# Performance work log

Hardware: AMD Instinct MI355X
Metric: run time of the kernel (lower is better)

Reference implementation:

```python
import jax, jax.numpy as jnp
import numpy as np

N = 20000
E = 320000
D_IN = 3
HID = 256
HEADS = 4
C = HID // HEADS  # per-head channels = 64
LAYERS = 3
NUM_GRAPHS = 64
LN_EPS = 1e-5
NEG_SLOPE = 0.2


def setup_inputs() -> dict:
    key = jax.random.key(0)
    ks = jax.random.split(key, 12)
    x = jax.random.normal(ks[0], (N, D_IN), dtype=jnp.float32)
    edge_index = jax.random.randint(ks[1], (2, E), 0, N, dtype=jnp.int64)
    batch = jnp.sort(jax.random.randint(ks[2], (N,), 0, NUM_GRAPHS, dtype=jnp.int64))
    s = 0.05
    W_emb = jax.random.normal(ks[3], (D_IN, HID), dtype=jnp.float32) * s
    b_emb = jnp.zeros((HID,), dtype=jnp.float32)
    W_gat = jax.random.normal(ks[4], (LAYERS, HID, HID), dtype=jnp.float32) * s
    att_src = jax.random.normal(ks[5], (LAYERS, HEADS, C), dtype=jnp.float32) * s
    att_dst = jax.random.normal(ks[6], (LAYERS, HEADS, C), dtype=jnp.float32) * s
    b_gat = jnp.zeros((LAYERS, HID), dtype=jnp.float32)
    ln_g = jnp.ones((LAYERS, HID), dtype=jnp.float32)
    ln_b = jnp.zeros((LAYERS, HID), dtype=jnp.float32)
    return {"x": x, "edge_index": edge_index, "batch": batch,
            "W_emb": W_emb, "b_emb": b_emb, "W_gat": W_gat,
            "att_src": att_src, "att_dst": att_dst, "b_gat": b_gat,
            "ln_g": ln_g, "ln_b": ln_b}


def _layer_norm(h, g, b):
    mu = jnp.mean(h, axis=-1, keepdims=True)
    var = jnp.var(h, axis=-1, keepdims=True)
    return (h - mu) * jax.lax.rsqrt(var + LN_EPS) * g + b


def _gat_layer(h, src, dst, loop_mask, Wl, a_s, a_d, bl):
    # h: [N, HID] -> per-head features [N, H, C]
    hp = (h @ Wl).reshape(N, HEADS, C)
    alpha_s = jnp.einsum('nhc,hc->nh', hp, a_s)   # [N, H]
    alpha_d = jnp.einsum('nhc,hc->nh', hp, a_d)   # [N, H]
    # edges + self-loops; pre-existing self-loops masked out (PyG removes then re-adds)
    e = jax.nn.leaky_relu(alpha_s[src] + alpha_d[dst], NEG_SLOPE)  # [E+N, H]
    e = jnp.where(loop_mask[:, None], -jnp.inf, e)
    # segment softmax over destination neighborhoods
    m = jax.ops.segment_max(e, dst, num_segments=N)
    ex = jnp.exp(e - m[dst])
    denom = jax.ops.segment_sum(ex, dst, num_segments=N)
    alpha = ex / jnp.maximum(denom[dst], 1e-16)    # [E+N, H]
    # weighted scatter-add of source features
    out = jax.ops.segment_sum(alpha[:, :, None] * hp[src], dst, num_segments=N)  # [N,H,C]
    return out.reshape(N, HID) + bl, alpha


def reference(x, edge_index, batch, W_emb, b_emb, W_gat, att_src, att_dst, b_gat, ln_g, ln_b):
    src0 = edge_index[0]
    dst0 = edge_index[1]
    loop_ids = jnp.arange(N, dtype=src0.dtype)
    src = jnp.concatenate([src0, loop_ids])
    dst = jnp.concatenate([dst0, loop_ids])
    loop_mask = jnp.concatenate([src0 == dst0, jnp.zeros((N,), dtype=bool)])

    h = x @ W_emb + b_emb  # node embedding
    attns = []
    for l in range(LAYERS):
        h, alpha = _gat_layer(h, src, dst, loop_mask, W_gat[l], att_src[l], att_dst[l], b_gat[l])
        h = _layer_norm(h, ln_g[l], ln_b[l])
        attns.append(alpha)
        # dropout is identity in eval mode
    # global mean pool over graphs
    sums = jax.ops.segment_sum(h, batch, num_segments=NUM_GRAPHS)
    cnts = jax.ops.segment_sum(jnp.ones((N,), dtype=h.dtype), batch, num_segments=NUM_GRAPHS)
    graph_repr = sums / jnp.maximum(cnts, 1.0)[:, None]
    return h, graph_repr, jnp.stack(attns)
```

## Files before the change

### kernel.cpp

```cpp
#include <hip/hip_runtime.h>
#include <hip/hip_bf16.h>

#define N_NODES 20000
#define E_EDGES 320000
#define HID 256
#define HEADS 4
#define CPH 64
#define LAYERS 3
#define NGRAPH 64
#define LN_EPS 1e-5f
#define NEG 0.2f
#define MAXD 256

__device__ __forceinline__ float lrelu_f(float v){ return v > 0.f ? v : NEG*v; }

__global__ __launch_bounds__(256) void k_cvt_f(const int* __restrict__ raw,
                                               int* __restrict__ src, int* __restrict__ dst){
  int e = blockIdx.x*256 + threadIdx.x;
  if (e >= E_EDGES) return;
  src[e] = raw[e];
  dst[e] = raw[E_EDGES + e];
}

__global__ __launch_bounds__(256) void k_embed_f(const float* __restrict__ x, const float* __restrict__ W,
                                                 const float* __restrict__ b, float* __restrict__ h){
  int n = blockIdx.x; int c = threadIdx.x;
  float x0 = x[n*3+0], x1 = x[n*3+1], x2 = x[n*3+2];
  h[(size_t)n*HID+c] = fmaf(x0, W[c], fmaf(x1, W[HID+c], fmaf(x2, W[2*HID+c], b[c])));
}

__global__ void k_hist_f(const int* __restrict__ dst, int* __restrict__ deg){
  int e = blockIdx.x*256 + threadIdx.x;
  if (e < E_EDGES) atomicAdd(&deg[dst[e]], 1);
}

__global__ __launch_bounds__(256) void k_scan_f(const int* __restrict__ deg, int* __restrict__ rp, int* __restrict__ cur){
  __shared__ int part[256];
  const int CH = (N_NODES + 255)/256;
  int t = threadIdx.x;
  int s = 0;
  for (int i=0;i<CH;i++){ int idx=t*CH+i; if (idx<N_NODES) s += deg[idx]; }
  part[t]=s; __syncthreads();
  for (int off=1; off<256; off<<=1){
    int v = (t>=off) ? part[t-off] : 0; __syncthreads();
    part[t]+=v; __syncthreads();
  }
  int run = (t==0) ? 0 : part[t-1];
  for (int i=0;i<CH;i++){ int idx=t*CH+i; if (idx<N_NODES){ rp[idx]=run; cur[idx]=run; run+=deg[idx]; } }
  if (t==255) rp[N_NODES]=run;
}

__global__ void k_scatter_f(const int* __restrict__ src, const int* __restrict__ dst, int* __restrict__ cur,
                            int* __restrict__ csrc, int* __restrict__ ceid){
  int e = blockIdx.x*256 + threadIdx.x;
  if (e < E_EDGES){
    int d = dst[e];
    int pos = atomicAdd(&cur[d],1);
    csrc[pos] = src[e];
    ceid[pos] = e;
  }
}

__global__ __launch_bounds__(256) void k_gemm_f(const float* __restrict__ A, const float* __restrict__ B,
                                                float* __restrict__ C, int M){
  __shared__ float sA[64][68];
  __shared__ float sB[64][68];
  int r0 = blockIdx.x*64, c0 = blockIdx.y*64;
  int tid = threadIdx.x, tx = tid&15, ty = tid>>4;
  float acc[4][4] = {};
  for (int k0=0; k0<HID; k0+=64){
    #pragma unroll
    for (int i=0;i<4;i++){
      int slot = tid + i*256;
      int rr = slot>>4, kk = (slot&15)<<2;
      int gr = r0+rr; if (gr >= M) gr = M-1;
      float4 va = *(const float4*)(A + (size_t)gr*HID + k0 + kk);
      sA[kk+0][rr]=va.x; sA[kk+1][rr]=va.y; sA[kk+2][rr]=va.z; sA[kk+3][rr]=va.w;
      float4 vb = *(const float4*)(B + (size_t)(k0+rr)*HID + c0 + kk);
      sB[rr][kk+0]=vb.x; sB[rr][kk+1]=vb.y; sB[rr][kk+2]=vb.z; sB[rr][kk+3]=vb.w;
    }
    __syncthreads();
    #pragma unroll 8
    for (int k=0;k<64;k++){
      float4 a4 = *(const float4*)&sA[k][ty*4];
      float4 b4 = *(const float4*)&sB[k][tx*4];
      float av[4]={a4.x,a4.y,a4.z,a4.w}, bv[4]={b4.x,b4.y,b4.z,b4.w};
      #pragma unroll
      for (int i=0;i<4;i++)
        #pragma unroll
        for (int j=0;j<4;j++) acc[i][j] = fmaf(av[i], bv[j], acc[i][j]);
    }
    __syncthreads();
  }
  #pragma unroll
  for (int i=0;i<4;i++){
    int r = r0 + ty*4 + i;
    if (r < M){
      float4 o = {acc[i][0],acc[i][1],acc[i][2],acc[i][3]};
      *(float4*)(C + (size_t)r*HID + c0 + tx*4) = o;
    }
  }
}

__global__ __launch_bounds__(64) void k_alpha_f(const float* __restrict__ hp, const float* __restrict__ as_w,
                                                const float* __restrict__ ad_w,
                                                float* __restrict__ asn, float* __restrict__ adn){
  int n = blockIdx.x, lane = threadIdx.x;
  #pragma unroll
  for (int h=0; h<HEADS; h++){
    float v = hp[(size_t)n*HID + h*CPH + lane];
    float ps = v * as_w[h*CPH + lane];
    float pd = v * ad_w[h*CPH + lane];
    #pragma unroll
    for (int off=32; off; off>>=1){ ps += __shfl_xor(ps, off, 64); pd += __shfl_xor(pd, off, 64); }
    if (lane == 0){ asn[n*HEADS+h] = ps; adn[n*HEADS+h] = pd; }
  }
}

__global__ __launch_bounds__(64) void k_aggr_f(const float* __restrict__ hp, const float* __restrict__ asn,
                                               const float* __restrict__ adn, const int* __restrict__ rp,
                                               const int* __restrict__ csrc, const int* __restrict__ ceid,
                                               const float* __restrict__ bl, const float* __restrict__ lg,
                                               const float* __restrict__ lb, float* __restrict__ hout,
                                               float* __restrict__ attn,
                                               float* __restrict__ hOut32){
  __shared__ float ps[MAXD][HEADS];
  int n = blockIdx.x, lane = threadIdx.x;
  int beg = rp[n];
  int cnt = rp[n+1] - beg;
  float ad[HEADS], es[HEADS];
  #pragma unroll
  for (int h=0;h<HEADS;h++){
    ad[h]=adn[n*HEADS+h];
    es[h]=lrelu_f(asn[n*HEADS+h]+ad[h]);
  }
  float dp[HEADS] = {0.f,0.f,0.f,0.f};
  for (int j=lane; j<cnt; j+=64){
    int s = csrc[beg+j];
    #pragma unroll
    for (int h=0;h<HEADS;h++){
      float p = 0.f;
      if (s != n) p = __expf(lrelu_f(asn[s*HEADS+h]+ad[h]));
      if (j < MAXD) ps[j][h] = p;
      dp[h] += p;
    }
  }
  #pragma unroll
  for (int h=0;h<HEADS;h++){
    #pragma unroll
    for (int off=32; off; off>>=1) dp[h] += __shfl_xor(dp[h], off, 64);
  }
  float slf[HEADS], inv[HEADS];
  #pragma unroll
  for (int h=0;h<HEADS;h++){
    slf[h] = __expf(es[h]);
    inv[h] = 1.f / fmaxf(dp[h] + slf[h], 1e-16f);
  }
  __syncthreads();
  for (int j=lane; j<cnt; j+=64){
    int s = csrc[beg+j];
    size_t eid = (size_t)ceid[beg+j];
    #pragma unroll
    for (int h=0;h<HEADS;h++){
      float p = (j < MAXD) ? ps[j][h]
              : ((s!=n) ? __expf(lrelu_f(asn[s*HEADS+h]+ad[h])) : 0.f);
      attn[eid*HEADS + h] = p * inv[h];
    }
  }
  if (lane==0){
    #pragma unroll
    for (int h=0;h<HEADS;h++)
      attn[(size_t)(E_EDGES+n)*HEADS + h] = slf[h]*inv[h];
  }
  float acc[HEADS];
  #pragma unroll
  for (int h=0;h<HEADS;h++) acc[h] = slf[h]*hp[(size_t)n*HID + h*CPH + lane];
  for (int j=0;j<cnt;j++){
    int s = csrc[beg+j];
    if (j < MAXD){
      #pragma unroll
      for (int h=0;h<HEADS;h++)
        acc[h] = fmaf(ps[j][h], hp[(size_t)s*HID + h*CPH + lane], acc[h]);
    } else if (s != n){
      #pragma unroll
      for (int h=0;h<HEADS;h++){
        float p = __expf(lrelu_f(asn[s*HEADS+h]+ad[h]));
        acc[h] = fmaf(p, hp[(size_t)s*HID + h*CPH + lane], acc[h]);
      }
    }
  }
  float o[HEADS], sum=0.f, sq=0.f;
  #pragma unroll
  for (int h=0;h<HEADS;h++){
    o[h] = fmaf(acc[h], inv[h], bl[h*CPH+lane]);
    sum += o[h]; sq = fmaf(o[h],o[h],sq);
  }
  #pragma unroll
  for (int off=32; off; off>>=1){ sum += __shfl_xor(sum,off,64); sq += __shfl_xor(sq,off,64); }
  float mu = sum * (1.f/HID);
  float var = sq*(1.f/HID) - mu*mu;
  float rs = rsqrtf(var + LN_EPS);
  #pragma unroll
  for (int h=0;h<HEADS;h++){
    int c = h*CPH+lane;
    float y = (o[h]-mu)*rs*lg[c] + lb[c];
    hout[(size_t)n*HID + c] = y;
    if (hOut32) hOut32[(size_t)n*HID + c] = y;
  }
}

__global__ __launch_bounds__(256) void k_pool1(const float* __restrict__ h, const int* __restrict__ batch,
                                               float* __restrict__ gracc){
  const int nb = 2048;
  const int chunk = (N_NODES + nb - 1)/nb;
  int n0 = blockIdx.x*chunk;
  int n1 = n0 + chunk; if (n1 > N_NODES) n1 = N_NODES;
  if (n0 >= n1) return;
  int c = threadIdx.x;
  float acc = 0.f; int curg = -1;
  for (int n=n0; n<n1; ++n){
    int g = batch[n];
    if (g != curg){
      if (curg >= 0) atomicAdd(&gracc[curg*HID+c], acc);
      curg = g; acc = 0.f;
    }
    acc += h[(size_t)n*HID + c];
  }
  if (curg >= 0) atomicAdd(&gracc[curg*HID+c], acc);
}

__global__ __launch_bounds__(256) void k_pool2(const float* __restrict__ gracc, const int* __restrict__ batch,
                                               float* __restrict__ out_gr){
  int g = blockIdx.x, c = threadIdx.x;
  int lo=0, hi=N_NODES;
  while (lo<hi){ int mid=(lo+hi)>>1; if (batch[mid] < g) lo=mid+1; else hi=mid; }
  int start = lo;
  lo=start; hi=N_NODES;
  while (lo<hi){ int mid=(lo+hi)>>1; if (batch[mid] < g+1) lo=mid+1; else hi=mid; }
  float cnt = (float)(lo - start);
  out_gr[g*HID + c] = gracc[g*HID + c] / fmaxf(cnt, 1.f);
}

extern "C" void kernel_launch(void* const* d_in, const int* in_sizes, int n_in,
                              void* d_out, int out_size, void* d_ws, size_t ws_size,
                              hipStream_t stream){
  const float* x     = (const float*)d_in[0];
  const int*   ei    = (const int*)d_in[1];
  const int*   batch = (const int*)d_in[2];
  const float* W_emb = (const float*)d_in[3];
  const float* b_emb = (const float*)d_in[4];
  const float* W_gat = (const float*)d_in[5];
  const float* att_s = (const float*)d_in[6];
  const float* att_d = (const float*)d_in[7];
  const float* b_gat = (const float*)d_in[8];
  const float* ln_g  = (const float*)d_in[9];
  const float* ln_b  = (const float*)d_in[10];

  float* out     = (float*)d_out;
  float* out_h   = out;
  float* out_gr  = out + (size_t)N_NODES*HID;
  float* out_att = out_gr + (size_t)NGRAPH*HID;

  char* ws = (char*)d_ws;
  size_t off = 0;
  auto alloc = [&](size_t bytes){ void* p = ws + off; off += (bytes + 255) & ~size_t(255); return p; };
  float* h_cur = (float*)alloc((size_t)N_NODES*HID*4);
  float* hp    = (float*)alloc((size_t)N_NODES*HID*4);
  float* asn   = (float*)alloc((size_t)N_NODES*HEADS*4);
  float* adn   = (float*)alloc((size_t)N_NODES*HEADS*4);
  int* deg     = (int*)alloc((size_t)N_NODES*4);
  int* rp      = (int*)alloc((size_t)(N_NODES+1)*4);
  int* cur     = (int*)alloc((size_t)N_NODES*4);
  int* csrc    = (int*)alloc((size_t)E_EDGES*4);
  int* ceid    = (int*)alloc((size_t)E_EDGES*4);
  int* srcA    = (int*)alloc((size_t)E_EDGES*4);
  int* dstA    = (int*)alloc((size_t)E_EDGES*4);
  float* gracc = (float*)alloc((size_t)NGRAPH*HID*4);

  hipMemsetAsync(deg, 0, (size_t)N_NODES*4, stream);
  hipMemsetAsync(gracc, 0, (size_t)NGRAPH*HID*4, stream);

  k_cvt_f    <<<(E_EDGES+255)/256, 256, 0, stream>>>(ei, srcA, dstA);
  k_hist_f   <<<(E_EDGES+255)/256, 256, 0, stream>>>(dstA, deg);
  k_scan_f   <<<1, 256, 0, stream>>>(deg, rp, cur);
  k_scatter_f<<<(E_EDGES+255)/256, 256, 0, stream>>>(srcA, dstA, cur, csrc, ceid);

  k_embed_f  <<<N_NODES, 256, 0, stream>>>(x, W_emb, b_emb, h_cur);

  dim3 ggrid((N_NODES+63)/64, HID/64);
  for (int l=0; l<LAYERS; ++l){
    k_gemm_f <<<ggrid, 256, 0, stream>>>(h_cur, W_gat + (size_t)l*HID*HID, hp, N_NODES);
    k_alpha_f<<<N_NODES, 64, 0, stream>>>(hp, att_s + l*HEADS*CPH, att_d + l*HEADS*CPH, asn, adn);
    k_aggr_f <<<N_NODES, 64, 0, stream>>>(hp, asn, adn, rp, csrc, ceid,
              b_gat + l*HID, ln_g + l*HID, ln_b + l*HID, h_cur,
              out_att + (size_t)l*(E_EDGES+N_NODES)*HEADS,
              (l==LAYERS-1) ? out_h : (float*)nullptr);
  }
  k_pool1<<<2048, 256, 0, stream>>>(h_cur, batch, gracc);
  k_pool2<<<NGRAPH, 256, 0, stream>>>(gracc, batch, out_gr);
}
```

Measured before the change: 494.2 us.

## Split aggregation across four wavefronts and write attention in a separate edge-order kernel

The per-node aggregation kernel now runs 256 threads (four wavefronts), with each wavefront handling a strided subset of neighbours. Partial sums and the softmax denominator are combined through shared memory, and layer norm is applied with one channel per thread. Per-edge attention output is no longer scattered by edge id from CSR order. The kernel instead stores per-node inverse denominators, and a new coalesced edge-order kernel recomputes alpha and writes float4 rows, which removes the ceid array. The cost is an extra kernel launch per layer and recomputing exp for every edge, plus additional syncthreads.

```diff
diff --git a/kernel.cpp b/kernel.cpp
--- a/kernel.cpp
+++ b/kernel.cpp
@@ -51,13 +51,12 @@
 }
 
 __global__ void k_scatter_f(const int* __restrict__ src, const int* __restrict__ dst, int* __restrict__ cur,
-                            int* __restrict__ csrc, int* __restrict__ ceid){
+                            int* __restrict__ csrc){
   int e = blockIdx.x*256 + threadIdx.x;
   if (e < E_EDGES){
     int d = dst[e];
     int pos = atomicAdd(&cur[d],1);
     csrc[pos] = src[e];
-    ceid[pos] = e;
   }
 }
 
@@ -117,25 +116,29 @@
   }
 }
 
-__global__ __launch_bounds__(64) void k_aggr_f(const float* __restrict__ hp, const float* __restrict__ asn,
-                                               const float* __restrict__ adn, const int* __restrict__ rp,
-                                               const int* __restrict__ csrc, const int* __restrict__ ceid,
-                                               const float* __restrict__ bl, const float* __restrict__ lg,
-                                               const float* __restrict__ lb, float* __restrict__ hout,
-                                               float* __restrict__ attn,
-                                               float* __restrict__ hOut32){
-  __shared__ float ps[MAXD][HEADS];
-  int n = blockIdx.x, lane = threadIdx.x;
+__global__ __launch_bounds__(256) void k_aggr_f(const float* __restrict__ hp, const float* __restrict__ asn,
+                                                const float* __restrict__ adn, const int* __restrict__ rp,
+                                                const int* __restrict__ csrc,
+                                                const float* __restrict__ bl, const float* __restrict__ lg,
+                                                const float* __restrict__ lb, float* __restrict__ hout,
+                                                float* __restrict__ invg, float* __restrict__ attn,
+                                                float* __restrict__ hOut32){
+  __shared__ float ps[MAXD][5];
+  __shared__ float pacc[4][256];
+  __shared__ float wden[4][4];
+  __shared__ float wsum[4], wsq[4];
+  int n = blockIdx.x, t = threadIdx.x;
+  int w = t>>6, l = t&63;
   int beg = rp[n];
   int cnt = rp[n+1] - beg;
-  float ad[HEADS], es[HEADS];
+  float ad[HEADS], slf[HEADS];
   #pragma unroll
   for (int h=0;h<HEADS;h++){
     ad[h]=adn[n*HEADS+h];
-    es[h]=lrelu_f(asn[n*HEADS+h]+ad[h]);
+    slf[h]=__expf(lrelu_f(asn[n*HEADS+h]+ad[h]));
   }
   float dp[HEADS] = {0.f,0.f,0.f,0.f};
-  for (int j=lane; j<cnt; j+=64){
+  for (int j=t; j<cnt; j+=256){
     int s = csrc[beg+j];
     #pragma unroll
     for (int h=0;h<HEADS;h++){
@@ -150,63 +153,76 @@
     #pragma unroll
     for (int off=32; off; off>>=1) dp[h] += __shfl_xor(dp[h], off, 64);
   }
-  float slf[HEADS], inv[HEADS];
-  #pragma unroll
-  for (int h=0;h<HEADS;h++){
-    slf[h] = __expf(es[h]);
-    inv[h] = 1.f / fmaxf(dp[h] + slf[h], 1e-16f);
+  if (l==0){
+    #pragma unroll
+    for (int h=0;h<HEADS;h++) wden[w][h]=dp[h];
   }
   __syncthreads();
-  for (int j=lane; j<cnt; j+=64){
-    int s = csrc[beg+j];
-    size_t eid = (size_t)ceid[beg+j];
+  float inv[HEADS];
+  #pragma unroll
+  for (int h=0;h<HEADS;h++)
+    inv[h] = 1.f / fmaxf(wden[0][h]+wden[1][h]+wden[2][h]+wden[3][h] + slf[h], 1e-16f);
+  if (t==0){
     #pragma unroll
     for (int h=0;h<HEADS;h++){
-      float p = (j < MAXD) ? ps[j][h]
-              : ((s!=n) ? __expf(lrelu_f(asn[s*HEADS+h]+ad[h])) : 0.f);
-      attn[eid*HEADS + h] = p * inv[h];
-    }
-  }
-  if (lane==0){
-    #pragma unroll
-    for (int h=0;h<HEADS;h++)
+      invg[n*HEADS+h] = inv[h];
       attn[(size_t)(E_EDGES+n)*HEADS + h] = slf[h]*inv[h];
-  }
-  float acc[HEADS];
-  #pragma unroll
-  for (int h=0;h<HEADS;h++) acc[h] = slf[h]*hp[(size_t)n*HID + h*CPH + lane];
-  for (int j=0;j<cnt;j++){
+    }
+  }
+  float acc[HEADS] = {0.f,0.f,0.f,0.f};
+  for (int j=w; j<cnt; j+=4){
     int s = csrc[beg+j];
     if (j < MAXD){
       #pragma unroll
       for (int h=0;h<HEADS;h++)
-        acc[h] = fmaf(ps[j][h], hp[(size_t)s*HID + h*CPH + lane], acc[h]);
+        acc[h] = fmaf(ps[j][h], hp[(size_t)s*HID + h*CPH + l], acc[h]);
     } else if (s != n){
       #pragma unroll
       for (int h=0;h<HEADS;h++){
         float p = __expf(lrelu_f(asn[s*HEADS+h]+ad[h]));
-        acc[h] = fmaf(p, hp[(size_t)s*HID + h*CPH + lane], acc[h]);
+        acc[h] = fmaf(p, hp[(size_t)s*HID + h*CPH + l], acc[h]);
       }
     }
   }
-  float o[HEADS], sum=0.f, sq=0.f;
+  if (w==0){
+    #pragma unroll
+    for (int h=0;h<HEADS;h++)
+      acc[h] = fmaf(slf[h], hp[(size_t)n*HID + h*CPH + l], acc[h]);
+  }
+  #pragma unroll
+  for (int h=0;h<HEADS;h++) pacc[w][h*CPH + l] = acc[h];
+  __syncthreads();
+  float o = (pacc[0][t]+pacc[1][t]+pacc[2][t]+pacc[3][t]) * inv[t>>6] + bl[t];
+  float sum = o, sq = o*o;
+  #pragma unroll
+  for (int off=32; off; off>>=1){ sum += __shfl_xor(sum,off,64); sq += __shfl_xor(sq,off,64); }
+  if (l==0){ wsum[w]=sum; wsq[w]=sq; }
+  __syncthreads();
+  float S = wsum[0]+wsum[1]+wsum[2]+wsum[3];
+  float Q = wsq[0]+wsq[1]+wsq[2]+wsq[3];
+  float mu = S * (1.f/HID);
+  float var = Q*(1.f/HID) - mu*mu;
+  float rs = rsqrtf(var + LN_EPS);
+  float y = (o-mu)*rs*lg[t] + lb[t];
+  hout[(size_t)n*HID + t] = y;
+  if (hOut32) hOut32[(size_t)n*HID + t] = y;
+}
+
+__global__ __launch_bounds__(256) void k_attn(const int* __restrict__ srcA, const int* __restrict__ dstA,
+                                              const float* __restrict__ asn, const float* __restrict__ adn,
+                                              const float* __restrict__ invg, float* __restrict__ attn){
+  int e = blockIdx.x*256 + threadIdx.x;
+  if (e >= E_EDGES) return;
+  int s = srcA[e], d = dstA[e];
+  float4 o;
+  float* po = (float*)&o;
   #pragma unroll
   for (int h=0;h<HEADS;h++){
-    o[h] = fmaf(acc[h], inv[h], bl[h*CPH+lane]);
-    sum += o[h]; sq = fmaf(o[h],o[h],sq);
-  }
-  #pragma unroll
-  for (int off=32; off; off>>=1){ sum += __shfl_xor(sum,off,64); sq += __shfl_xor(sq,off,64); }
-  float mu = sum * (1.f/HID);
-  float var = sq*(1.f/HID) - mu*mu;
-  float rs = rsqrtf(var + LN_EPS);
-  #pragma unroll
-  for (int h=0;h<HEADS;h++){
-    int c = h*CPH+lane;
-    float y = (o[h]-mu)*rs*lg[c] + lb[c];
-    hout[(size_t)n*HID + c] = y;
-    if (hOut32) hOut32[(size_t)n*HID + c] = y;
-  }
+    float a = 0.f;
+    if (s != d) a = __expf(lrelu_f(asn[s*HEADS+h]+adn[d*HEADS+h])) * invg[d*HEADS+h];
+    po[h] = a;
+  }
+  *(float4*)(attn + (size_t)e*HEADS) = o;
 }
 
 __global__ __launch_bounds__(256) void k_pool1(const float* __restrict__ h, const int* __restrict__ batch,
@@ -268,11 +284,11 @@
   float* hp    = (float*)alloc((size_t)N_NODES*HID*4);
   float* asn   = (float*)alloc((size_t)N_NODES*HEADS*4);
   float* adn   = (float*)alloc((size_t)N_NODES*HEADS*4);
+  float* invg  = (float*)alloc((size_t)N_NODES*HEADS*4);
   int* deg     = (int*)alloc((size_t)N_NODES*4);
   int* rp      = (int*)alloc((size_t)(N_NODES+1)*4);
   int* cur     = (int*)alloc((size_t)N_NODES*4);
   int* csrc    = (int*)alloc((size_t)E_EDGES*4);
-  int* ceid    = (int*)alloc((size_t)E_EDGES*4);
   int* srcA    = (int*)alloc((size_t)E_EDGES*4);
   int* dstA    = (int*)alloc((size_t)E_EDGES*4);
   float* gracc = (float*)alloc((size_t)NGRAPH*HID*4);
@@ -280,21 +296,24 @@
   hipMemsetAsync(deg, 0, (size_t)N_NODES*4, stream);
   hipMemsetAsync(gracc, 0, (size_t)NGRAPH*HID*4, stream);
 
-  k_cvt_f    <<<(E_EDGES+255)/256, 256, 0, stream>>>(ei, srcA, dstA);
-  k_hist_f   <<<(E_EDGES+255)/256, 256, 0, stream>>>(dstA, deg);
+  const int EG = (E_EDGES+255)/256;
+  k_cvt_f    <<<EG, 256, 0, stream>>>(ei, srcA, dstA);
+  k_hist_f   <<<EG, 256, 0, stream>>>(dstA, deg);
   k_scan_f   <<<1, 256, 0, stream>>>(deg, rp, cur);
-  k_scatter_f<<<(E_EDGES+255)/256, 256, 0, stream>>>(srcA, dstA, cur, csrc, ceid);
+  k_scatter_f<<<EG, 256, 0, stream>>>(srcA, dstA, cur, csrc);
 
   k_embed_f  <<<N_NODES, 256, 0, stream>>>(x, W_emb, b_emb, h_cur);
 
   dim3 ggrid((N_NODES+63)/64, HID/64);
   for (int l=0; l<LAYERS; ++l){
+    float* attn_l = out_att + (size_t)l*(E_EDGES+N_NODES)*HEADS;
     k_gemm_f <<<ggrid, 256, 0, stream>>>(h_cur, W_gat + (size_t)l*HID*HID, hp, N_NODES);
     k_alpha_f<<<N_NODES, 64, 0, stream>>>(hp, att_s + l*HEADS*CPH, att_d + l*HEADS*CPH, asn, adn);
-    k_aggr_f <<<N_NODES, 64, 0, stream>>>(hp, asn, adn, rp, csrc, ceid,
+    k_aggr_f <<<N_NODES, 256, 0, stream>>>(hp, asn, adn, rp, csrc,
               b_gat + l*HID, ln_g + l*HID, ln_b + l*HID, h_cur,
-              out_att + (size_t)l*(E_EDGES+N_NODES)*HEADS,
+              invg, attn_l,
               (l==LAYERS-1) ? out_h : (float*)nullptr);
+    k_attn   <<<EG, 256, 0, stream>>>(srcA, dstA, asn, adn, invg, attn_l);
   }
   k_pool1<<<2048, 256, 0, stream>>>(h_cur, batch, gracc);
   k_pool2<<<NGRAPH, 256, 0, stream>>>(gracc, batch, out_gr);
```

Result: slower. 611.3 us (+23.7%).
